# Kernel optimization log

Hardware: AMD Instinct MI355X
Metric: run time of the kernel (lower is better)

Reference implementation:

```python
import jax, jax.numpy as jnp
import numpy as np

D_MODEL = 1024
D_FF = 4096
N = 16384


def setup_inputs() -> dict:
    key = jax.random.key(0)
    k_b, k_w1, k_b1, k_w2, k_b2 = jax.random.split(key, 5)
    s1 = 1.0 / np.sqrt(D_MODEL)
    s2 = 1.0 / np.sqrt(D_FF)
    return {
        "batch": jax.random.normal(k_b, (N, D_MODEL), dtype=jnp.float32),
        # nn.Linear stores weight as [out_features, in_features]
        "W1": jax.random.uniform(k_w1, (D_FF, D_MODEL), jnp.float32, -s1, s1),
        "b1": jax.random.uniform(k_b1, (D_FF,), jnp.float32, -s1, s1),
        "W2": jax.random.uniform(k_w2, (D_MODEL, D_FF), jnp.float32, -s2, s2),
        "b2": jax.random.uniform(k_b2, (D_MODEL,), jnp.float32, -s2, s2),
    }


def reference(batch, W1, b1, W2, b2):
    # inner = tanh(linear1(batch)) : [N, d_ff]
    inner = jnp.tanh(batch @ W1.T + b1)
    # wx = tanh(linear2(inner)) : [N, d_model]
    wx = jnp.tanh(inner @ W2.T + b2)
    # diag(wx @ batch.T) == row-wise dot product, avoids O(N^2) matmul
    return jax.nn.sigmoid(jnp.sum(wx * batch, axis=-1))  # [N]
```

## Files before the change

### kernel.cpp

```cpp
#include <hip/hip_runtime.h>
#include <math.h>

#define N_ROWS 16384
#define DMODEL 1024
#define DFF    4096

typedef _Float16 f16;
typedef __attribute__((ext_vector_type(4))) _Float16 f16x4;
typedef __attribute__((ext_vector_type(8))) _Float16 f16x8;
typedef __attribute__((ext_vector_type(4))) float f32x4;

__device__ inline void async_ld16(const f16* g, f16* l) {
  __builtin_amdgcn_global_load_lds(
      (__attribute__((address_space(1))) void*)(g),
      (__attribute__((address_space(3))) void*)(l),
      16, 0, 0);
}

__global__ void cast_to_f16(const float* __restrict__ src, f16* __restrict__ dst, int n) {
  int i = (blockIdx.x * blockDim.x + threadIdx.x) * 8;
  if (i >= n) return;
  float4 v0 = ((const float4*)(src + i))[0];
  float4 v1 = ((const float4*)(src + i))[1];
  f16x8 h = { (f16)v0.x, (f16)v0.y, (f16)v0.z, (f16)v0.w,
              (f16)v1.x, (f16)v1.y, (f16)v1.z, (f16)v1.w };
  *(f16x8*)(dst + i) = h;
}

template <int K, typename OUT_T>
__global__ __launch_bounds__(256, 3)
void gemm_bt_tanh(const f16* __restrict__ A, const f16* __restrict__ B,
                  const float* __restrict__ bias, OUT_T* __restrict__ C, int Nc) {
  __shared__ __align__(16) f16 As[128 * 32];
  __shared__ __align__(16) f16 Bs[128 * 32];

  const int tid  = threadIdx.x;
  const int lane = tid & 63;
  const int wave = tid >> 6;
  const size_t row0 = (size_t)blockIdx.x * 128;
  const size_t col0 = (size_t)blockIdx.y * 128;
  const int wm = (wave >> 1) * 64;
  const int wn = (wave & 1) * 64;
  const int fr = lane & 15;
  const int fk = (lane >> 4) * 8;

  const int srow   = tid >> 2;
  const int schunk = (tid & 3) * 8;
  const f16* Ap = A + (row0 + srow) * (size_t)K + schunk;
  const f16* Bp = B + (col0 + srow) * (size_t)K + schunk;
  f16* Asd = As + tid * 8;
  f16* Bsd = Bs + tid * 8;

  f32x4 acc[4][4] = {};

  for (int k0 = 0; k0 < K; k0 += 32) {
    __syncthreads();
    async_ld16(Ap + k0, Asd);
    async_ld16(Ap + (size_t)64 * K + k0, Asd + 2048);
    async_ld16(Bp + k0, Bsd);
    async_ld16(Bp + (size_t)64 * K + k0, Bsd + 2048);
    __syncthreads();

    f16x8 af[4], bf[4];
#pragma unroll
    for (int i = 0; i < 4; ++i) {
      af[i] = *(const f16x8*)(As + (wm + i * 16 + fr) * 32 + fk);
      bf[i] = *(const f16x8*)(Bs + (wn + i * 16 + fr) * 32 + fk);
    }
#pragma unroll
    for (int i = 0; i < 4; ++i)
#pragma unroll
      for (int j = 0; j < 4; ++j)
        acc[i][j] = __builtin_amdgcn_mfma_f32_16x16x32_f16(af[i], bf[j], acc[i][j], 0, 0, 0);
  }

  const int erow = wm + (lane >> 4) * 4;
  const int ecol = wn + fr;
#pragma unroll
  for (int i = 0; i < 4; ++i) {
#pragma unroll
    for (int j = 0; j < 4; ++j) {
      size_t gcol = col0 + ecol + j * 16;
      float b = bias[gcol];
#pragma unroll
      for (int r = 0; r < 4; ++r) {
        size_t grow = row0 + erow + i * 16 + r;
        C[grow * (size_t)Nc + gcol] = (OUT_T)tanhf(acc[i][j][r] + b);
      }
    }
  }
}

__global__ void rowdot_sigmoid(const f16* __restrict__ wx, const float* __restrict__ batch,
                               float* __restrict__ out) {
  const int row = blockIdx.x;
  const int t = threadIdx.x;
  const f16* wr = wx + (size_t)row * DMODEL + t * 4;
  const float* br = batch + (size_t)row * DMODEL + t * 4;
  f16x4 h = *(const f16x4*)wr;
  float4 b4 = *(const float4*)br;
  float s = (float)h[0] * b4.x + (float)h[1] * b4.y + (float)h[2] * b4.z + (float)h[3] * b4.w;
#pragma unroll
  for (int off = 32; off > 0; off >>= 1) s += __shfl_down(s, off, 64);
  __shared__ float partial[4];
  if ((t & 63) == 0) partial[t >> 6] = s;
  __syncthreads();
  if (t == 0) {
    float tot = partial[0] + partial[1] + partial[2] + partial[3];
    out[row] = 1.0f / (1.0f + expf(-tot));
  }
}

extern "C" void kernel_launch(void* const* d_in, const int* in_sizes, int n_in,
                              void* d_out, int out_size, void* d_ws, size_t ws_size,
                              hipStream_t stream) {
  const float* batch = (const float*)d_in[0];
  const float* W1    = (const float*)d_in[1];
  const float* b1    = (const float*)d_in[2];
  const float* W2    = (const float*)d_in[3];
  const float* b2    = (const float*)d_in[4];
  float* out = (float*)d_out;

  char* ws = (char*)d_ws;
  f16* batch_h = (f16*)ws;  ws += (size_t)N_ROWS * DMODEL * sizeof(f16);
  f16* W1_h    = (f16*)ws;  ws += (size_t)DFF * DMODEL * sizeof(f16);
  f16* W2_h    = (f16*)ws;  ws += (size_t)DMODEL * DFF * sizeof(f16);
  f16* inner_h = (f16*)ws;  ws += (size_t)N_ROWS * DFF * sizeof(f16);
  f16* wx_h    = (f16*)ws;  ws += (size_t)N_ROWS * DMODEL * sizeof(f16);

  const int nb  = N_ROWS * DMODEL;
  const int nw  = DFF * DMODEL;
  cast_to_f16<<<nb / 2048, 256, 0, stream>>>(batch, batch_h, nb);
  cast_to_f16<<<nw / 2048, 256, 0, stream>>>(W1, W1_h, nw);
  cast_to_f16<<<nw / 2048, 256, 0, stream>>>(W2, W2_h, nw);

  dim3 g1(N_ROWS / 128, DFF / 128);
  gemm_bt_tanh<DMODEL, f16><<<g1, 256, 0, stream>>>(batch_h, W1_h, b1, inner_h, DFF);
  dim3 g2(N_ROWS / 128, DMODEL / 128);
  gemm_bt_tanh<DFF, f16><<<g2, 256, 0, stream>>>(inner_h, W2_h, b2, wx_h, DMODEL);

  rowdot_sigmoid<<<N_ROWS, 256, 0, stream>>>(wx_h, batch, out);
}
```

Baseline: 487.9 us.

## Swizzle LDS tiles and fuse row-dot into second GEMM epilogue

Applies an XOR swizzle to the LDS chunk layout in both GEMMs so fragment reads hit fewer bank conflicts. It also fuses the tanh(wx)·batch row dot product into the second GEMM's epilogue, using shuffle reductions and float atomicAdd into a per-row buffer. A final small sigmoid kernel replaces the separate rowdot pass. This removes the wx round trip through global memory and one kernel launch, at the cost of atomics across 8 column blocks, uncoalesced fp32 batch reads in the epilogue, and two extra tiny kernels.

After: 566.6 us. 16.1% more time.

```diff
diff --git a/kernel.cpp b/kernel.cpp
--- a/kernel.cpp
+++ b/kernel.cpp
@@ -27,10 +27,21 @@
   *(f16x8*)(dst + i) = h;
 }
 
-template <int K, typename OUT_T>
+__global__ void zero_f32(float* __restrict__ p, int n) {
+  int i = blockIdx.x * blockDim.x + threadIdx.x;
+  if (i < n) p[i] = 0.0f;
+}
+
+__global__ void sigmoid_f32(const float* __restrict__ pre, float* __restrict__ out, int n) {
+  int i = blockIdx.x * blockDim.x + threadIdx.x;
+  if (i < n) out[i] = 1.0f / (1.0f + expf(-pre[i]));
+}
+
+
+template <int K>
 __global__ __launch_bounds__(256, 3)
 void gemm_bt_tanh(const f16* __restrict__ A, const f16* __restrict__ B,
-                  const float* __restrict__ bias, OUT_T* __restrict__ C, int Nc) {
+                  const float* __restrict__ bias, f16* __restrict__ C, int Nc) {
   __shared__ __align__(16) f16 As[128 * 32];
   __shared__ __align__(16) f16 Bs[128 * 32];
 
@@ -42,10 +53,10 @@
   const int wm = (wave >> 1) * 64;
   const int wn = (wave & 1) * 64;
   const int fr = lane & 15;
-  const int fk = (lane >> 4) * 8;
+  const int swz = (((lane >> 4) ^ (fr >> 2)) * 8);
 
   const int srow   = tid >> 2;
-  const int schunk = (tid & 3) * 8;
+  const int schunk = (((tid & 3) ^ ((tid >> 4) & 3)) * 8);
   const f16* Ap = A + (row0 + srow) * (size_t)K + schunk;
   const f16* Bp = B + (col0 + srow) * (size_t)K + schunk;
   f16* Asd = As + tid * 8;
@@ -64,8 +75,8 @@
     f16x8 af[4], bf[4];
 #pragma unroll
     for (int i = 0; i < 4; ++i) {
-      af[i] = *(const f16x8*)(As + (wm + i * 16 + fr) * 32 + fk);
-      bf[i] = *(const f16x8*)(Bs + (wn + i * 16 + fr) * 32 + fk);
+      af[i] = *(const f16x8*)(As + (wm + i * 16 + fr) * 32 + swz);
+      bf[i] = *(const f16x8*)(Bs + (wn + i * 16 + fr) * 32 + swz);
     }
 #pragma unroll
     for (int i = 0; i < 4; ++i)
@@ -85,29 +96,89 @@
 #pragma unroll
       for (int r = 0; r < 4; ++r) {
         size_t grow = row0 + erow + i * 16 + r;
-        C[grow * (size_t)Nc + gcol] = (OUT_T)tanhf(acc[i][j][r] + b);
+        C[grow * (size_t)Nc + gcol] = (f16)tanhf(acc[i][j][r] + b);
       }
     }
   }
 }
 
-__global__ void rowdot_sigmoid(const f16* __restrict__ wx, const float* __restrict__ batch,
-                               float* __restrict__ out) {
-  const int row = blockIdx.x;
-  const int t = threadIdx.x;
-  const f16* wr = wx + (size_t)row * DMODEL + t * 4;
-  const float* br = batch + (size_t)row * DMODEL + t * 4;
-  f16x4 h = *(const f16x4*)wr;
-  float4 b4 = *(const float4*)br;
-  float s = (float)h[0] * b4.x + (float)h[1] * b4.y + (float)h[2] * b4.z + (float)h[3] * b4.w;
-#pragma unroll
-  for (int off = 32; off > 0; off >>= 1) s += __shfl_down(s, off, 64);
-  __shared__ float partial[4];
-  if ((t & 63) == 0) partial[t >> 6] = s;
-  __syncthreads();
-  if (t == 0) {
-    float tot = partial[0] + partial[1] + partial[2] + partial[3];
-    out[row] = 1.0f / (1.0f + expf(-tot));
+template <int K>
+__global__ __launch_bounds__(256, 3)
+void gemm_bt_tanh_dot(const f16* __restrict__ A, const f16* __restrict__ B,
+                      const float* __restrict__ bias,
+                      const float* __restrict__ batch,
+                      float* __restrict__ pre) {
+  __shared__ __align__(16) f16 As[128 * 32];
+  __shared__ __align__(16) f16 Bs[128 * 32];
+
+  const int tid  = threadIdx.x;
+  const int lane = tid & 63;
+  const int wave = tid >> 6;
+  const size_t row0 = (size_t)blockIdx.x * 128;
+  const size_t col0 = (size_t)blockIdx.y * 128;
+  const int wm = (wave >> 1) * 64;
+  const int wn = (wave & 1) * 64;
+  const int fr = lane & 15;
+  const int swz = (((lane >> 4) ^ (fr >> 2)) * 8);
+
+  const int srow   = tid >> 2;
+  const int schunk = (((tid & 3) ^ ((tid >> 4) & 3)) * 8);
+  const f16* Ap = A + (row0 + srow) * (size_t)K + schunk;
+  const f16* Bp = B + (col0 + srow) * (size_t)K + schunk;
+  f16* Asd = As + tid * 8;
+  f16* Bsd = Bs + tid * 8;
+
+  f32x4 acc[4][4] = {};
+
+  for (int k0 = 0; k0 < K; k0 += 32) {
+    __syncthreads();
+    async_ld16(Ap + k0, Asd);
+    async_ld16(Ap + (size_t)64 * K + k0, Asd + 2048);
+    async_ld16(Bp + k0, Bsd);
+    async_ld16(Bp + (size_t)64 * K + k0, Bsd + 2048);
+    __syncthreads();
+
+    f16x8 af[4], bf[4];
+#pragma unroll
+    for (int i = 0; i < 4; ++i) {
+      af[i] = *(const f16x8*)(As + (wm + i * 16 + fr) * 32 + swz);
+      bf[i] = *(const f16x8*)(Bs + (wn + i * 16 + fr) * 32 + swz);
+    }
+#pragma unroll
+    for (int i = 0; i < 4; ++i)
+#pragma unroll
+      for (int j = 0; j < 4; ++j)
+        acc[i][j] = __builtin_amdgcn_mfma_f32_16x16x32_f16(af[i], bf[j], acc[i][j], 0, 0, 0);
+  }
+
+  const int erow = wm + (lane >> 4) * 4;
+  const int ecol = wn + fr;
+  float psum[4][4] = {};
+#pragma unroll
+  for (int j = 0; j < 4; ++j) {
+    size_t gcol = col0 + ecol + j * 16;
+    float b = bias[gcol];
+#pragma unroll
+    for (int i = 0; i < 4; ++i) {
+#pragma unroll
+      for (int r = 0; r < 4; ++r) {
+        size_t grow = row0 + erow + i * 16 + r;
+        float w = tanhf(acc[i][j][r] + b);
+        psum[i][r] += w * batch[grow * (size_t)DMODEL + gcol];
+      }
+    }
+  }
+#pragma unroll
+  for (int i = 0; i < 4; ++i) {
+#pragma unroll
+    for (int r = 0; r < 4; ++r) {
+      float s = psum[i][r];
+      s += __shfl_xor(s, 1, 64);
+      s += __shfl_xor(s, 2, 64);
+      s += __shfl_xor(s, 4, 64);
+      s += __shfl_xor(s, 8, 64);
+      if (fr == 0) atomicAdd(&pre[row0 + erow + i * 16 + r], s);
+    }
   }
 }
 
@@ -126,18 +197,19 @@
   f16* W1_h    = (f16*)ws;  ws += (size_t)DFF * DMODEL * sizeof(f16);
   f16* W2_h    = (f16*)ws;  ws += (size_t)DMODEL * DFF * sizeof(f16);
   f16* inner_h = (f16*)ws;  ws += (size_t)N_ROWS * DFF * sizeof(f16);
-  f16* wx_h    = (f16*)ws;  ws += (size_t)N_ROWS * DMODEL * sizeof(f16);
-
-  const int nb  = N_ROWS * DMODEL;
-  const int nw  = DFF * DMODEL;
+  float* pre   = (float*)ws; ws += (size_t)N_ROWS * sizeof(float);
+
+  const int nb = N_ROWS * DMODEL;
+  const int nw = DFF * DMODEL;
+  zero_f32<<<N_ROWS / 256, 256, 0, stream>>>(pre, N_ROWS);
   cast_to_f16<<<nb / 2048, 256, 0, stream>>>(batch, batch_h, nb);
   cast_to_f16<<<nw / 2048, 256, 0, stream>>>(W1, W1_h, nw);
   cast_to_f16<<<nw / 2048, 256, 0, stream>>>(W2, W2_h, nw);
 
   dim3 g1(N_ROWS / 128, DFF / 128);
-  gemm_bt_tanh<DMODEL, f16><<<g1, 256, 0, stream>>>(batch_h, W1_h, b1, inner_h, DFF);
+  gemm_bt_tanh<DMODEL><<<g1, 256, 0, stream>>>(batch_h, W1_h, b1, inner_h, DFF);
   dim3 g2(N_ROWS / 128, DMODEL / 128);
-  gemm_bt_tanh<DFF, f16><<<g2, 256, 0, stream>>>(inner_h, W2_h, b2, wx_h, DMODEL);
-
-  rowdot_sigmoid<<<N_ROWS, 256, 0, stream>>>(wx_h, batch, out);
-}
+  gemm_bt_tanh_dot<DFF><<<g2, 256, 0, stream>>>(inner_h, W2_h, b2, batch, pre);
+
+  sigmoid_f32<<<N_ROWS / 256, 256, 0, stream>>>(pre, out, N_ROWS);
+}
```
